# Kernel tuning notes

Measured on AMD Instinct MI355X. Metric: run time of the kernel, lower is better.

Reference implementation:

```python
import jax, jax.numpy as jnp
import numpy as np

B, S, D = 4, 2048, 1024
E, ES, K = 16, 256, 4  # n_experts, expert_size, top-k (= n_heads)
STD_GATE = 0.02


def setup_inputs() -> dict:
    key = jax.random.key(0)
    k1, k2, k3, k4 = jax.random.split(key, 4)
    x = jax.random.normal(k1, (B, S, D), dtype=jnp.float32)
    # init per module: gate ~ N(0, d^-0.5), keys ~ N(0, d^-0.5), values ~ N(0, size^-0.5)
    w_gate = jax.random.normal(k2, (E, D), dtype=jnp.float32) * (D ** -0.5)
    keys = jax.random.normal(k3, (E, D, ES), dtype=jnp.float32) * (D ** -0.5)
    values = jax.random.normal(k4, (E, ES, D), dtype=jnp.float32) * ((E * ES) ** -0.5)
    return {"x": x, "w_gate": w_gate, "keys": keys, "values": values}


def reference(x, w_gate, keys, values):
    # sigma-MoE forward (selection_mode='sigmoid', activation=relu,
    # num_selected = n_heads = K, no bias, no dropout, eval mode)
    xt = x.reshape(-1, D)                         # [T, D]
    T = xt.shape[0]
    logits = xt @ w_gate.T                        # [T, E]
    sel = jax.nn.sigmoid(logits)                  # sigmoid gating
    sel_val, sel_idx = jax.lax.top_k(sel, K)      # [T, K]
    # sparse gate weights as dense [T, E] mask (zeros for unselected experts)
    gate_w = jnp.zeros((T, E), dtype=x.dtype).at[
        jnp.arange(T)[:, None], sel_idx
    ].set(sel_val)
    # per-expert hidden: h[t,e,s] = relu(sum_d x[t,d] keys[e,d,s])
    h = jax.nn.relu(jnp.einsum('td,eds->tes', xt, keys))  # [T, E, ES]
    # weighted scatter back through values: out = sum_e gate * h_e @ values_e
    out = jnp.einsum('tes,te,esv->tv', h, gate_w, values)  # [T, D]
    return out.reshape(B, S, D)
```

## Files before the change

### kernel.cpp

```cpp
#include <hip/hip_runtime.h>
#include <hip/hip_bf16.h>
#include <stdint.h>

#define T_TOK 8192
#define DIM   1024
#define NEXP  16
#define ESZ   256
#define TOPK  4
#define BM    64
#define BK    64
#define NPAIR (T_TOK*TOPK)
#define NBLK  128
#define MAXROWS (NPAIR + NEXP*BM)
#define MAXTILES (NPAIR/BM + NEXP)

typedef __hip_bfloat16 bf16;
typedef short bf16x8 __attribute__((ext_vector_type(8)));
typedef float f32x4 __attribute__((ext_vector_type(4)));

__device__ __forceinline__ unsigned short f2bu(float f){
  __hip_bfloat16 b = __float2bfloat16(f);
  return *reinterpret_cast<unsigned short*>(&b);
}
__device__ __forceinline__ float bu2f(unsigned short u){
  __hip_bfloat16 b = *reinterpret_cast<__hip_bfloat16*>(&u);
  return __bfloat162float(b);
}

__device__ __forceinline__ void gload16(const void* g, void* l){
  __builtin_amdgcn_global_load_lds((const __attribute__((address_space(1))) void*)g,
                                   (__attribute__((address_space(3))) void*)l, 16, 0, 0);
}

__global__ __launch_bounds__(256) void k_gate_dot(const float* __restrict__ x,
    const float* __restrict__ wg, bf16* __restrict__ xb, float* __restrict__ plog)
{
  __shared__ float wlds[NEXP*512];
  const int tid = threadIdx.x;
  const int half = blockIdx.x & 1;
  const int tg   = blockIdx.x >> 1;

  {
    const float4* src = (const float4*)wg;
    float4* dst = (float4*)wlds;
#pragma unroll
    for (int i=0;i<8;i++){
      int idx = tid + i*256;
      int e = idx >> 7, d4 = idx & 127;
      dst[idx] = src[e*256 + half*128 + d4];
    }
  }
  __syncthreads();

  const int ts = tid >> 5;
  const int dc = tid & 31;
  const int t0 = tg*16 + ts, t1 = t0 + 8;
  const float* xr0 = x + (size_t)t0*DIM + half*512;
  const float* xr1 = x + (size_t)t1*DIM + half*512;
  unsigned short* xd0 = (unsigned short*)xb + (size_t)t0*DIM + half*512;
  unsigned short* xd1 = (unsigned short*)xb + (size_t)t1*DIM + half*512;

  float acc0[NEXP], acc1[NEXP];
#pragma unroll
  for (int e=0;e<NEXP;e++){ acc0[e]=0.f; acc1[e]=0.f; }

#pragma unroll
  for (int i=0;i<4;i++){
    const int d0 = i*128 + dc*4;
    float4 xv0 = *(const float4*)(xr0 + d0);
    float4 xv1 = *(const float4*)(xr1 + d0);
    ushort4 o0; o0.x=f2bu(xv0.x); o0.y=f2bu(xv0.y); o0.z=f2bu(xv0.z); o0.w=f2bu(xv0.w);
    ushort4 o1; o1.x=f2bu(xv1.x); o1.y=f2bu(xv1.y); o1.z=f2bu(xv1.z); o1.w=f2bu(xv1.w);
    *(ushort4*)(xd0 + d0) = o0;
    *(ushort4*)(xd1 + d0) = o1;
#pragma unroll
    for (int e=0;e<NEXP;e++){
      float4 w = *(const float4*)(wlds + e*512 + d0);
      acc0[e] += xv0.x*w.x + xv0.y*w.y + xv0.z*w.z + xv0.w*w.w;
      acc1[e] += xv1.x*w.x + xv1.y*w.y + xv1.z*w.z + xv1.w*w.w;
    }
  }

#pragma unroll
  for (int e=0;e<NEXP;e++){
#pragma unroll
    for (int s=1;s<32;s<<=1){
      acc0[e] += __shfl_xor(acc0[e], s);
      acc1[e] += __shfl_xor(acc1[e], s);
    }
  }

  if (dc==0){
    float* p0 = plog + (size_t)t0*32 + half*16;
    float* p1 = plog + (size_t)t1*32 + half*16;
#pragma unroll
    for (int i=0;i<4;i++){
      f32x4 v0 = {acc0[i*4],acc0[i*4+1],acc0[i*4+2],acc0[i*4+3]};
      f32x4 v1 = {acc1[i*4],acc1[i*4+1],acc1[i*4+2],acc1[i*4+3]};
      *(f32x4*)(p0 + i*4) = v0;
      *(f32x4*)(p1 + i*4) = v1;
    }
  }
}

__global__ __launch_bounds__(256) void k_gate_top4(const float* __restrict__ plog,
    int* __restrict__ sel_idx, float* __restrict__ sel_gate,
    int* __restrict__ block_hist)
{
  __shared__ int h[4][NEXP];
  const int tid = threadIdx.x;
  if (tid < 64) h[tid>>4][tid&15] = 0;
  __syncthreads();

  const int t = blockIdx.x*256 + tid;
  const float* p = plog + (size_t)t*32;
  float v[NEXP];
#pragma unroll
  for (int i=0;i<4;i++){
    f32x4 a = *(const f32x4*)(p + i*4);
    f32x4 b = *(const f32x4*)(p + 16 + i*4);
#pragma unroll
    for (int j=0;j<4;j++) v[i*4+j] = 1.f/(1.f + expf(-(a[j]+b[j])));
  }
#pragma unroll
  for (int k=0;k<TOPK;k++){
    float bv=-2.f; int bi=0;
#pragma unroll
    for (int e=0;e<NEXP;e++) if (v[e] > bv){ bv=v[e]; bi=e; }
    sel_idx[t*TOPK+k]=bi; sel_gate[t*TOPK+k]=bv;
    atomicAdd(&h[tid>>6][bi],1);
    v[bi] = -2.f;
  }
  __syncthreads();
  if (tid < 64)
    block_hist[((size_t)blockIdx.x*4 + (tid>>4))*NEXP + (tid&15)] = h[tid>>4][tid&15];
}

__global__ __launch_bounds__(256) void k_transpose2(const float* __restrict__ keys,
    const float* __restrict__ values, bf16* __restrict__ kT, bf16* __restrict__ vT)
{
  __shared__ float tile[32][33];
  const int which = blockIdx.y >> 4, e = blockIdx.y & 15;
  const int R = which ? ESZ : DIM, C = which ? DIM : ESZ;
  const float* src = (which ? values : keys) + (size_t)e*DIM*ESZ;
  bf16* dst = (which ? vT : kT) + (size_t)e*DIM*ESZ;
  const int ctiles = C/32;
  const int r0 = (blockIdx.x / ctiles)*32, c0 = (blockIdx.x % ctiles)*32;
  const int tx = threadIdx.x & 31, ty = threadIdx.x >> 5;
#pragma unroll
  for (int i=0;i<4;i++){ int r = ty + i*8; tile[r][tx] = src[(size_t)(r0+r)*C + c0 + tx]; }
  __syncthreads();
#pragma unroll
  for (int i=0;i<4;i++){ int r = ty + i*8; dst[(size_t)(c0+r)*R + r0 + tx] = __float2bfloat16(tile[tx][r]); }
}

__global__ void k_meta(const int* __restrict__ gh,
    int* __restrict__ tile_expert, int* __restrict__ tile_rowstart,
    int* __restrict__ tile_segend, int* __restrict__ block_base)
{
  __shared__ int sbc[NBLK][NEXP];
  __shared__ int cnt[NEXP], seg[NEXP];
  const int tid = threadIdx.x;
  for (int cell = tid; cell < NBLK*NEXP; cell += 256)
    sbc[cell>>4][cell&15] = gh[cell];
  __syncthreads();
  if (tid < NEXP){
    int s=0;
    for (int sb=0; sb<NBLK; sb++) s += sbc[sb][tid];
    cnt[tid]=s;
  }
  __syncthreads();
  if (tid==0){
    int off=0, tc=0;
    for (int e=0;e<NEXP;e++){
      seg[e]=off;
      int c = cnt[e];
      int nt = (c + BM - 1)/BM;
      for (int i=0;i<nt;i++){
        tile_expert[tc]=e; tile_rowstart[tc]=off+i*BM; tile_segend[tc]=off+c; tc++;
      }
      off += nt*BM;
    }
    for (; tc<MAXTILES; tc++) tile_expert[tc]=-1;
  }
  __syncthreads();
  if (tid < NEXP){
    int s = seg[tid];
    for (int sb=0; sb<NBLK; sb++){ block_base[sb*NEXP + tid] = s; s += sbc[sb][tid]; }
  }
}

__global__ __launch_bounds__(256) void k_scatter(const int* __restrict__ sel_idx,
    const float* __restrict__ sel_gate, const int* __restrict__ block_base,
    int* __restrict__ assign_token, float* __restrict__ assign_gate,
    int* __restrict__ inv_rows)
{
  __shared__ int wcnt[4][NEXP];
  const int p = blockIdx.x*256 + threadIdx.x;
  const int wave = threadIdx.x >> 6, lane = threadIdx.x & 63;
  const int e = sel_idx[p];
  const float g = sel_gate[p];
  int rank = 0;
#pragma unroll
  for (int ee=0; ee<NEXP; ee++){
    unsigned long long m = __ballot(e==ee);
    if (lane==0) wcnt[wave][ee] = (int)__popcll(m);
    if (e==ee) rank = (int)__popcll(m & ((1ull<<lane)-1ull));
  }
  __syncthreads();
  int pre = 0;
  for (int w=0; w<wave; w++) pre += wcnt[w][e];
  const int row = block_base[blockIdx.x*NEXP + e] + pre + rank;
  assign_token[row] = p >> 2;
  assign_gate[row]  = g;
  inv_rows[p] = row;
}

__global__ __launch_bounds__(256) void k_gemm1(
    const bf16* __restrict__ xb, const bf16* __restrict__ kT,
    const int* __restrict__ assign_token, const float* __restrict__ assign_gate,
    const int* __restrict__ tile_expert, const int* __restrict__ tile_rowstart,
    const int* __restrict__ tile_segend, bf16* __restrict__ h)
{
  __shared__ char smem[49152];
  __shared__ int   tokens_s[BM];
  __shared__ float gates_s[BM];

  const int nb = blockIdx.x, tile = blockIdx.y;
  const int e = tile_expert[tile];
  if (e < 0) return;
  const int row0 = tile_rowstart[tile];
  const int segend = tile_segend[tile];
  const int tid = threadIdx.x, wave = tid>>6, lane = tid&63;

  if (tid < BM){
    int rg = row0 + tid;
    bool vld = rg < segend;
    tokens_s[tid] = vld ? assign_token[rg] : 0;
    gates_s[tid]  = vld ? assign_gate[rg] : 0.f;
  }
  __syncthreads();

  const bf16* qA[2]; const bf16* qB[4]; int loA[2], loB[4];
#pragma unroll
  for (int i=0;i<2;i++){
    int row = i*32 + wave*8 + (lane>>3);
    int c   = (lane&7) ^ (row&7);
    qA[i] = xb + (size_t)tokens_s[row]*DIM + c*8;
    loA[i] = i*4096 + wave*1024;
  }
#pragma unroll
  for (int i=0;i<4;i++){
    int col = i*32 + wave*8 + (lane>>3);
    int c   = (lane&7) ^ (col&7);
    qB[i] = kT + ((size_t)e*ESZ + nb*128 + col)*DIM + c*8;
    loB[i] = i*4096 + wave*1024;
  }

  const int wr0 = (wave>>1)*32, wc0 = (wave&1)*64;
  int offA[2][2], offB[2][4];
#pragma unroll
  for (int kk=0;kk<2;kk++){
    int kb = kk*64 + (lane>>4)*16;
#pragma unroll
    for (int m=0;m<2;m++){ int row = wr0 + m*16 + (lane&15); offA[kk][m] = row*128 + (kb ^ ((row&7)<<4)); }
#pragma unroll
    for (int n=0;n<4;n++){ int col = wc0 + n*16 + (lane&15); offB[kk][n] = col*128 + (kb ^ ((col&7)<<4)); }
  }

  f32x4 acc[2][4];
#pragma unroll
  for (int m=0;m<2;m++)
#pragma unroll
    for (int n=0;n<4;n++) acc[m][n] = {0.f,0.f,0.f,0.f};

  auto stage = [&](int abase, int bbase){
#pragma unroll
    for (int i=0;i<2;i++){ gload16(qA[i], smem + abase + loA[i]); qA[i]+=BK; }
#pragma unroll
    for (int i=0;i<4;i++){ gload16(qB[i], smem + bbase + loB[i]); qB[i]+=BK; }
  };
  auto compute = [&](const char* Ab, const char* Bb){
#pragma unroll
    for (int kk=0;kk<2;kk++){
      bf16x8 af[2], bfr[4];
#pragma unroll
      for (int m=0;m<2;m++) af[m]  = *(const bf16x8*)(Ab + offA[kk][m]);
#pragma unroll
      for (int n=0;n<4;n++) bfr[n] = *(const bf16x8*)(Bb + offB[kk][n]);
#pragma unroll
      for (int m=0;m<2;m++)
#pragma unroll
        for (int n=0;n<4;n++)
          acc[m][n] = __builtin_amdgcn_mfma_f32_16x16x32_bf16(af[m], bfr[n], acc[m][n], 0,0,0);
    }
  };

  stage(0, 16384);
  asm volatile("s_waitcnt vmcnt(0)" ::: "memory");
  __builtin_amdgcn_s_barrier();

  for (int kt=0; kt<16; kt+=2){
    stage(8192, 32768);
    compute(smem, smem+16384);
    asm volatile("s_waitcnt vmcnt(0)" ::: "memory");
    __builtin_amdgcn_s_barrier();
    if (kt+2 < 16) stage(0, 16384);
    compute(smem+8192, smem+32768);
    asm volatile("s_waitcnt vmcnt(0)" ::: "memory");
    __builtin_amdgcn_s_barrier();
  }

#pragma unroll
  for (int m=0;m<2;m++)
#pragma unroll
    for (int n=0;n<4;n++){
      int col = wc0 + n*16 + (lane&15);
#pragma unroll
      for (int j=0;j<4;j++){
        int rloc = wr0 + m*16 + ((lane>>4)<<2) + j;
        float v = fmaxf(acc[m][n][j], 0.f) * gates_s[rloc];
        h[(size_t)(row0 + rloc)*ESZ + nb*128 + col] = __float2bfloat16(v);
      }
    }
}

__global__ __launch_bounds__(256) void k_gemm2(
    const bf16* __restrict__ h, const bf16* __restrict__ vT,
    const int* __restrict__ tile_expert, const int* __restrict__ tile_rowstart,
    bf16* __restrict__ partial)
{
  __shared__ char smem[49152];

  const int nb = blockIdx.x, tile = blockIdx.y;
  const int e = tile_expert[tile];
  if (e < 0) return;
  const int row0 = tile_rowstart[tile];
  const int tid = threadIdx.x, wave = tid>>6, lane = tid&63;

  const bf16* qA[2]; const bf16* qB[4]; int loA[2], loB[4];
#pragma unroll
  for (int i=0;i<2;i++){
    int row = i*32 + wave*8 + (lane>>3);
    int c   = (lane&7) ^ (row&7);
    qA[i] = h + (size_t)(row0 + row)*ESZ + c*8;
    loA[i] = i*4096 + wave*1024;
  }
#pragma unroll
  for (int i=0;i<4;i++){
    int col = i*32 + wave*8 + (lane>>3);
    int c   = (lane&7) ^ (col&7);
    qB[i] = vT + ((size_t)e*DIM + nb*128 + col)*ESZ + c*8;
    loB[i] = i*4096 + wave*1024;
  }

  const int wr0 = (wave>>1)*32, wc0 = (wave&1)*64;
  int offA[2][2], offB[2][4];
#pragma unroll
  for (int kk=0;kk<2;kk++){
    int kb = kk*64 + (lane>>4)*16;
#pragma unroll
    for (int m=0;m<2;m++){ int row = wr0 + m*16 + (lane&15); offA[kk][m] = row*128 + (kb ^ ((row&7)<<4)); }
#pragma unroll
    for (int n=0;n<4;n++){ int col = wc0 + n*16 + (lane&15); offB[kk][n] = col*128 + (kb ^ ((col&7)<<4)); }
  }

  f32x4 acc[2][4];
#pragma unroll
  for (int m=0;m<2;m++)
#pragma unroll
    for (int n=0;n<4;n++) acc[m][n] = {0.f,0.f,0.f,0.f};

  auto stage = [&](int abase, int bbase){
#pragma unroll
    for (int i=0;i<2;i++){ gload16(qA[i], smem + abase + loA[i]); qA[i]+=BK; }
#pragma unroll
    for (int i=0;i<4;i++){ gload16(qB[i], smem + bbase + loB[i]); qB[i]+=BK; }
  };
  auto compute = [&](const char* Ab, const char* Bb){
#pragma unroll
    for (int kk=0;kk<2;kk++){
      bf16x8 af[2], bfr[4];
#pragma unroll
      for (int m=0;m<2;m++) af[m]  = *(const bf16x8*)(Ab + offA[kk][m]);
#pragma unroll
      for (int n=0;n<4;n++) bfr[n] = *(const bf16x8*)(Bb + offB[kk][n]);
#pragma unroll
      for (int m=0;m<2;m++)
#pragma unroll
        for (int n=0;n<4;n++)
          acc[m][n] = __builtin_amdgcn_mfma_f32_16x16x32_bf16(af[m], bfr[n], acc[m][n], 0,0,0);
    }
  };

  stage(0, 16384);
  asm volatile("s_waitcnt vmcnt(0)" ::: "memory");
  __builtin_amdgcn_s_barrier();

  stage(8192, 32768);
  compute(smem, smem+16384);
  asm volatile("s_waitcnt vmcnt(0)" ::: "memory");
  __builtin_amdgcn_s_barrier();
  stage(0, 16384);
  compute(smem+8192, smem+32768);
  asm volatile("s_waitcnt vmcnt(0)" ::: "memory");
  __builtin_amdgcn_s_barrier();
  stage(8192, 32768);
  compute(smem, smem+16384);
  asm volatile("s_waitcnt vmcnt(0)" ::: "memory");
  __builtin_amdgcn_s_barrier();
  compute(smem+8192, smem+32768);

#pragma unroll
  for (int m=0;m<2;m++)
#pragma unroll
    for (int n=0;n<4;n++){
      int col = wc0 + n*16 + (lane&15);
#pragma unroll
      for (int j=0;j<4;j++){
        int rloc = wr0 + m*16 + ((lane>>4)<<2) + j;
        partial[(size_t)(row0 + rloc)*DIM + nb*128 + col] = __float2bfloat16(acc[m][n][j]);
      }
    }
}

__global__ __launch_bounds__(256) void k_reduce(const bf16* __restrict__ partial,
    const int* __restrict__ inv_rows, float* __restrict__ out)
{
  const int t = blockIdx.x;
  const int c0 = threadIdx.x * 4;
  int rows[TOPK];
#pragma unroll
  for (int k=0;k<TOPK;k++) rows[k] = inv_rows[t*TOPK+k];
  float a0=0.f,a1=0.f,a2=0.f,a3=0.f;
#pragma unroll
  for (int k=0;k<TOPK;k++){
    ushort4 v = *(const ushort4*)((const unsigned short*)partial + (size_t)rows[k]*DIM + c0);
    a0 += bu2f(v.x); a1 += bu2f(v.y); a2 += bu2f(v.z); a3 += bu2f(v.w);
  }
  float4 o = {a0,a1,a2,a3};
  *(float4*)(out + (size_t)t*DIM + c0) = o;
}

extern "C" void kernel_launch(void* const* d_in, const int* in_sizes, int n_in,
                              void* d_out, int out_size, void* d_ws, size_t ws_size,
                              hipStream_t stream)
{
  const float* x      = (const float*)d_in[0];
  const float* wg     = (const float*)d_in[1];
  const float* keys   = (const float*)d_in[2];
  const float* values = (const float*)d_in[3];
  float* out = (float*)d_out;

  char* ws = (char*)d_ws;
  size_t off = 0;
  bf16* vT   = (bf16*)(ws+off); off += (size_t)NEXP*DIM*ESZ*2;
  bf16* hbuf = (bf16*)(ws+off); off += (size_t)MAXROWS*ESZ*2;
  float* plog         = (float*)(ws+off); off += (size_t)T_TOK*32*4;
  int*   sel_idx      = (int*)  (ws+off); off += (size_t)NPAIR*4;
  float* sel_gate     = (float*)(ws+off); off += (size_t)NPAIR*4;
  int*   assign_token = (int*)  (ws+off); off += (size_t)MAXROWS*4;
  float* assign_gate  = (float*)(ws+off); off += (size_t)MAXROWS*4;
  int*   inv_rows     = (int*)  (ws+off); off += (size_t)NPAIR*4;
  int*   block_hist   = (int*)  (ws+off); off += (size_t)NBLK*NEXP*4;
  int*   block_base   = (int*)  (ws+off); off += (size_t)NBLK*NEXP*4;
  int*   tile_expert  = (int*)  (ws+off); off += 4096;
  int*   tile_rowstart= (int*)  (ws+off); off += 4096;
  int*   tile_segend  = (int*)  (ws+off); off += 4096;
  const size_t PARTIAL_BYTES = (size_t)MAXROWS*DIM*2;
  const size_t XB_BYTES = (size_t)T_TOK*DIM*2;
  const size_t KT_BYTES = (size_t)NEXP*ESZ*DIM*2;
  bf16* partial = (bf16*)(ws+off); off += PARTIAL_BYTES;
  bf16* xb = (bf16*)((char*)partial + PARTIAL_BYTES - XB_BYTES - KT_BYTES);
  bf16* kT = (bf16*)((char*)partial + PARTIAL_BYTES - KT_BYTES);

  k_gate_dot<<<T_TOK/16*2, 256, 0, stream>>>(x, wg, xb, plog);
  k_gate_top4<<<T_TOK/256, 256, 0, stream>>>(plog, sel_idx, sel_gate, block_hist);
  k_transpose2<<<dim3(256, NEXP*2), 256, 0, stream>>>(keys, values, kT, vT);
  k_meta<<<1, 256, 0, stream>>>(block_hist, tile_expert, tile_rowstart, tile_segend, block_base);
  k_scatter<<<NBLK, 256, 0, stream>>>(sel_idx, sel_gate, block_base, assign_token,
      assign_gate, inv_rows);
  k_gemm1<<<dim3(2, MAXTILES), 256, 0, stream>>>(xb, kT, assign_token, assign_gate,
      tile_expert, tile_rowstart, tile_segend, hbuf);
  k_gemm2<<<dim3(8, MAXTILES), 256, 0, stream>>>(hbuf, vT,
      tile_expert, tile_rowstart, partial);
  k_reduce<<<T_TOK, 256, 0, stream>>>(partial, inv_rows, out);
}
```

Measured before the change: 145.4 us.

## Shrink gemm1 N-tile to 64 and pipeline both GEMMs with partial vmcnt waits

In k_gemm1 the N tile drops from 128 to 64 columns, so the grid doubles in x, LDS per block falls to 32KB and each wave holds a 2x2 accumulator set. Both GEMM k-loops become a uniform double-buffered pipeline: the next stage is issued first, then the wait uses a partial vmcnt so the current buffer's loads finish while the next tile's loads stay in flight, instead of waiting for everything. The goal is more overlap of global loads with MFMA work and higher occupancy for gemm1. In exchange, A rows are reloaded twice as often and each wave has fewer MFMAs per LDS read.

Result: slower. 149.2 us (+2.6%).

```diff
diff --git a/kernel.cpp b/kernel.cpp
--- a/kernel.cpp
+++ b/kernel.cpp
@@ -222,7 +222,7 @@
     const int* __restrict__ tile_expert, const int* __restrict__ tile_rowstart,
     const int* __restrict__ tile_segend, bf16* __restrict__ h)
 {
-  __shared__ char smem[49152];
+  __shared__ char smem[32768];
   __shared__ int   tokens_s[BM];
   __shared__ float gates_s[BM];
 
@@ -241,86 +241,80 @@
   }
   __syncthreads();
 
-  const bf16* qA[2]; const bf16* qB[4]; int loA[2], loB[4];
+  const bf16* qA[2]; const bf16* qB[2]; int lo[2];
 #pragma unroll
   for (int i=0;i<2;i++){
     int row = i*32 + wave*8 + (lane>>3);
     int c   = (lane&7) ^ (row&7);
     qA[i] = xb + (size_t)tokens_s[row]*DIM + c*8;
-    loA[i] = i*4096 + wave*1024;
-  }
-#pragma unroll
-  for (int i=0;i<4;i++){
-    int col = i*32 + wave*8 + (lane>>3);
-    int c   = (lane&7) ^ (col&7);
-    qB[i] = kT + ((size_t)e*ESZ + nb*128 + col)*DIM + c*8;
-    loB[i] = i*4096 + wave*1024;
-  }
-
-  const int wr0 = (wave>>1)*32, wc0 = (wave&1)*64;
-  int offA[2][2], offB[2][4];
+    qB[i] = kT + ((size_t)e*ESZ + nb*64 + row)*DIM + c*8;
+    lo[i] = i*4096 + wave*1024;
+  }
+
+  const int wr0 = (wave>>1)*32, wc0 = (wave&1)*32;
+  int offA[2][2], offB[2][2];
 #pragma unroll
   for (int kk=0;kk<2;kk++){
     int kb = kk*64 + (lane>>4)*16;
 #pragma unroll
     for (int m=0;m<2;m++){ int row = wr0 + m*16 + (lane&15); offA[kk][m] = row*128 + (kb ^ ((row&7)<<4)); }
 #pragma unroll
-    for (int n=0;n<4;n++){ int col = wc0 + n*16 + (lane&15); offB[kk][n] = col*128 + (kb ^ ((col&7)<<4)); }
-  }
-
-  f32x4 acc[2][4];
+    for (int n=0;n<2;n++){ int col = wc0 + n*16 + (lane&15); offB[kk][n] = col*128 + (kb ^ ((col&7)<<4)); }
+  }
+
+  f32x4 acc[2][2];
 #pragma unroll
   for (int m=0;m<2;m++)
 #pragma unroll
-    for (int n=0;n<4;n++) acc[m][n] = {0.f,0.f,0.f,0.f};
+    for (int n=0;n<2;n++) acc[m][n] = {0.f,0.f,0.f,0.f};
 
   auto stage = [&](int abase, int bbase){
 #pragma unroll
-    for (int i=0;i<2;i++){ gload16(qA[i], smem + abase + loA[i]); qA[i]+=BK; }
-#pragma unroll
-    for (int i=0;i<4;i++){ gload16(qB[i], smem + bbase + loB[i]); qB[i]+=BK; }
+    for (int i=0;i<2;i++){ gload16(qA[i], smem + abase + lo[i]); qA[i]+=BK; }
+#pragma unroll
+    for (int i=0;i<2;i++){ gload16(qB[i], smem + bbase + lo[i]); qB[i]+=BK; }
   };
   auto compute = [&](const char* Ab, const char* Bb){
 #pragma unroll
     for (int kk=0;kk<2;kk++){
-      bf16x8 af[2], bfr[4];
+      bf16x8 af[2], bfr[2];
 #pragma unroll
       for (int m=0;m<2;m++) af[m]  = *(const bf16x8*)(Ab + offA[kk][m]);
 #pragma unroll
-      for (int n=0;n<4;n++) bfr[n] = *(const bf16x8*)(Bb + offB[kk][n]);
+      for (int n=0;n<2;n++) bfr[n] = *(const bf16x8*)(Bb + offB[kk][n]);
 #pragma unroll
       for (int m=0;m<2;m++)
 #pragma unroll
-        for (int n=0;n<4;n++)
+        for (int n=0;n<2;n++)
           acc[m][n] = __builtin_amdgcn_mfma_f32_16x16x32_bf16(af[m], bfr[n], acc[m][n], 0,0,0);
     }
   };
 
   stage(0, 16384);
-  asm volatile("s_waitcnt vmcnt(0)" ::: "memory");
-  __builtin_amdgcn_s_barrier();
-
-  for (int kt=0; kt<16; kt+=2){
-    stage(8192, 32768);
-    compute(smem, smem+16384);
-    asm volatile("s_waitcnt vmcnt(0)" ::: "memory");
+#pragma unroll
+  for (int kt=0; kt<16; ++kt){
+    const int cur = kt & 1;
+    if (kt < 15){
+      stage(cur ? 0 : 8192, cur ? 16384 : 24576);
+      asm volatile("s_waitcnt vmcnt(4)" ::: "memory");
+    } else {
+      asm volatile("s_waitcnt vmcnt(0)" ::: "memory");
+    }
     __builtin_amdgcn_s_barrier();
-    if (kt+2 < 16) stage(0, 16384);
-    compute(smem+8192, smem+32768);
-    asm volatile("s_waitcnt vmcnt(0)" ::: "memory");
+    compute(cur ? smem+8192 : smem, cur ? smem+24576 : smem+16384);
     __builtin_amdgcn_s_barrier();
   }
 
 #pragma unroll
   for (int m=0;m<2;m++)
 #pragma unroll
-    for (int n=0;n<4;n++){
+    for (int n=0;n<2;n++){
       int col = wc0 + n*16 + (lane&15);
 #pragma unroll
       for (int j=0;j<4;j++){
         int rloc = wr0 + m*16 + ((lane>>4)<<2) + j;
         float v = fmaxf(acc[m][n][j], 0.f) * gates_s[rloc];
-        h[(size_t)(row0 + rloc)*ESZ + nb*128 + col] = __float2bfloat16(v);
+        h[(size_t)(row0 + rloc)*ESZ + nb*64 + col] = __float2bfloat16(v);
       }
     }
 }
@@ -394,22 +388,19 @@
   };
 
   stage(0, 16384);
-  asm volatile("s_waitcnt vmcnt(0)" ::: "memory");
-  __builtin_amdgcn_s_barrier();
-
-  stage(8192, 32768);
-  compute(smem, smem+16384);
-  asm volatile("s_waitcnt vmcnt(0)" ::: "memory");
-  __builtin_amdgcn_s_barrier();
-  stage(0, 16384);
-  compute(smem+8192, smem+32768);
-  asm volatile("s_waitcnt vmcnt(0)" ::: "memory");
-  __builtin_amdgcn_s_barrier();
-  stage(8192, 32768);
-  compute(smem, smem+16384);
-  asm volatile("s_waitcnt vmcnt(0)" ::: "memory");
-  __builtin_amdgcn_s_barrier();
-  compute(smem+8192, smem+32768);
+#pragma unroll
+  for (int kt=0; kt<4; ++kt){
+    const int cur = kt & 1;
+    if (kt < 3){
+      stage(cur ? 0 : 8192, cur ? 16384 : 32768);
+      asm volatile("s_waitcnt vmcnt(6)" ::: "memory");
+    } else {
+      asm volatile("s_waitcnt vmcnt(0)" ::: "memory");
+    }
+    __builtin_amdgcn_s_barrier();
+    compute(cur ? smem+8192 : smem, cur ? smem+32768 : smem+16384);
+    __builtin_amdgcn_s_barrier();
+  }
 
 #pragma unroll
   for (int m=0;m<2;m++)
@@ -480,7 +471,7 @@
   k_meta<<<1, 256, 0, stream>>>(block_hist, tile_expert, tile_rowstart, tile_segend, block_base);
   k_scatter<<<NBLK, 256, 0, stream>>>(sel_idx, sel_gate, block_base, assign_token,
       assign_gate, inv_rows);
-  k_gemm1<<<dim3(2, MAXTILES), 256, 0, stream>>>(xb, kT, assign_token, assign_gate,
+  k_gemm1<<<dim3(4, MAXTILES), 256, 0, stream>>>(xb, kT, assign_token, assign_gate,
       tile_expert, tile_rowstart, tile_segend, hbuf);
   k_gemm2<<<dim3(8, MAXTILES), 256, 0, stream>>>(hbuf, vT,
       tile_expert, tile_rowstart, partial);
```
